# Performance work log

Hardware: AMD Instinct MI355X
Metric: run time of the kernel (lower is better)

The kernel has to match this reference:

```python
import jax, jax.numpy as jnp
import numpy as np

B, S, D_IN, D_OUT = 8, 1024, 4096, 4096

def setup_inputs() -> dict:
    key = jax.random.key(0)
    k_x, k_wp, k_wn = jax.random.split(key, 3)
    x = jax.random.normal(k_x, (B, S, D_IN), dtype=jnp.float32)
    # nn.Linear weights are [out_features, in_features]
    w_pos = jax.random.normal(k_wp, (D_OUT, D_IN), dtype=jnp.float32) * 0.02
    w_neg = jax.random.normal(k_wn, (D_OUT, D_IN), dtype=jnp.float32) * 0.02
    return {"x": x, "w_pos": w_pos, "w_neg": w_neg}

def reference(x, w_pos, w_neg):
    # Straight-through estimator quantization:
    #   w_pos_quant = (w_pos > 0).float(), gradient flows to w_pos
    #   w_neg_quant = -(w_neg <= 0).float(), gradient flows to w_neg
    wp_q = w_pos + jax.lax.stop_gradient((w_pos > 0).astype(w_pos.dtype) - w_pos)
    wn_q = w_neg + jax.lax.stop_gradient(-(w_neg <= 0).astype(w_neg.dtype) - w_neg)
    # F.linear(x, W) = x @ W.T ; two GEMMs summed
    y_pos = jnp.einsum('bsd,od->bso', x, wp_q)
    y_neg = jnp.einsum('bsd,od->bso', x, wn_q)
    return y_pos + y_neg
```

## Files before the change

kernel.cpp:

```cpp
#include <hip/hip_runtime.h>
#include <hip/hip_bf16.h>
#include <stdint.h>

#define M_TOT 8192
#define N_TOT 4096
#define K_TOT 4096

typedef __bf16 bf16x8 __attribute__((ext_vector_type(8)));
typedef float  f32x4  __attribute__((ext_vector_type(4)));

__device__ __forceinline__ uint16_t f2bf_rne(float f) {
  uint32_t u = __float_as_uint(f);
  u += 0x7fffu + ((u >> 16) & 1u);
  return (uint16_t)(u >> 16);
}

__device__ __forceinline__ uint32_t tern(float p, float n) {
  bool pp = p > 0.0f, nn = n > 0.0f;
  return pp ? (nn ? 0x3F80u : 0u) : (nn ? 0u : 0xBF80u);
}

__global__ __launch_bounds__(256) void cast_x_kernel(const float4* __restrict__ x,
                                                     uint4* __restrict__ out) {
  int t = blockIdx.x * 256 + threadIdx.x;
  float4 a = x[2 * t], b = x[2 * t + 1];
  uint4 o;
  o.x = (uint32_t)f2bf_rne(a.x) | ((uint32_t)f2bf_rne(a.y) << 16);
  o.y = (uint32_t)f2bf_rne(a.z) | ((uint32_t)f2bf_rne(a.w) << 16);
  o.z = (uint32_t)f2bf_rne(b.x) | ((uint32_t)f2bf_rne(b.y) << 16);
  o.w = (uint32_t)f2bf_rne(b.z) | ((uint32_t)f2bf_rne(b.w) << 16);
  out[t] = o;
}

__global__ __launch_bounds__(256) void ternarize_kernel(const float4* __restrict__ wp,
                                                        const float4* __restrict__ wn,
                                                        uint4* __restrict__ out) {
  int t = blockIdx.x * 256 + threadIdx.x;
  float4 p0 = wp[2 * t], p1 = wp[2 * t + 1];
  float4 n0 = wn[2 * t], n1 = wn[2 * t + 1];
  uint4 o;
  o.x = tern(p0.x, n0.x) | (tern(p0.y, n0.y) << 16);
  o.y = tern(p0.z, n0.z) | (tern(p0.w, n0.w) << 16);
  o.z = tern(p1.x, n1.x) | (tern(p1.y, n1.y) << 16);
  o.w = tern(p1.z, n1.z) | (tern(p1.w, n1.w) << 16);
  out[t] = o;
}


#define STAGE_HALF(SP0, SP1, DSTOFF)                                              \
  do {                                                                            \
    __builtin_amdgcn_global_load_lds(                                             \
        (const __attribute__((address_space(1))) unsigned int*)(SP0),             \
        (__attribute__((address_space(3))) unsigned int*)(smem + (DSTOFF) + lds0),\
        16, 0, 0);                                                                \
    __builtin_amdgcn_global_load_lds(                                             \
        (const __attribute__((address_space(1))) unsigned int*)(SP1),             \
        (__attribute__((address_space(3))) unsigned int*)(smem + (DSTOFF) + lds1),\
        16, 0, 0);                                                                \
  } while (0)

__global__ __launch_bounds__(512, 2) void gemm_tern_kernel(const uint16_t* __restrict__ Xb,
                                                           const uint16_t* __restrict__ Wb,
                                                           float* __restrict__ C) {
  __shared__ __align__(16) char smem[131072];
  const int tid  = threadIdx.x;
  const int wave = tid >> 6;
  const int lane = tid & 63;
  const int lh   = lane & 15, lq = lane >> 4;
  const int wm   = wave >> 2;
  const int wn   = wave & 3;

  const int id  = blockIdx.x;
  const int swz = (id & 7) * 64 + (id >> 3);
  const int bn  = swz & 15;
  const int bm  = swz >> 4;

  const int p16 = ((lq ^ ((lh >> 1) & 3)) << 4);
  int aoffs[8], boffs[4];
#pragma unroll
  for (int i = 0; i < 8; ++i) aoffs[i] = (wm * 128 + i * 16 + lh) * 64 + p16;
#pragma unroll
  for (int j = 0; j < 4; ++j) boffs[j] = 65536 + (wn * 64 + j * 16 + lh) * 64 + p16;

  const int lds0 = wave * 2048;
  const int lds1 = lds0 + 1024;
  const char *srcA0, *srcA1, *srcB0, *srcB1;
  {
    int o0 = lds0 + lane * 16, o1 = lds1 + lane * 16;
    int r0 = o0 >> 6, r1 = o1 >> 6;
    int c0 = ((o0 >> 4) & 3) ^ ((r0 >> 1) & 3);
    int c1 = ((o1 >> 4) & 3) ^ ((r1 >> 1) & 3);
    srcA0 = (const char*)Xb + (size_t)(bm * 256 + r0) * (K_TOT * 2) + c0 * 16;
    srcA1 = (const char*)Xb + (size_t)(bm * 256 + r1) * (K_TOT * 2) + c1 * 16;
    srcB0 = (const char*)Wb + (size_t)(bn * 256 + r0) * (K_TOT * 2) + c0 * 16;
    srcB1 = (const char*)Wb + (size_t)(bn * 256 + r1) * (K_TOT * 2) + c1 * 16;
  }

  f32x4 acc[8][4];
#pragma unroll
  for (int i = 0; i < 8; ++i)
#pragma unroll
    for (int j = 0; j < 4; ++j) acc[i][j] = (f32x4){0.f, 0.f, 0.f, 0.f};

  STAGE_HALF(srcA0, srcA1, 0);
  STAGE_HALF(srcB0, srcB1, 65536);
  STAGE_HALF(srcA0 + 64, srcA1 + 64, 32768);
  STAGE_HALF(srcB0 + 64, srcB1 + 64, 98304);
  STAGE_HALF(srcA0 + 128, srcA1 + 128, 16384);
  STAGE_HALF(srcB0 + 128, srcB1 + 128, 81920);
  asm volatile("s_waitcnt vmcnt(4)" ::: "memory");
  __builtin_amdgcn_s_barrier();
  asm volatile("" ::: "memory");

  for (int t = 0; t < 64; ++t) {
    const int curb = (t & 1) * 16384;
    const int nxtb = 16384 - curb;
    int offk1 = t * 128 + 192; if (offk1 > 8128) offk1 = 8128;
    int offk0 = t * 128 + 256; if (offk0 > 8128) offk0 = 8128;
    bf16x8 af[4], bfr[4];

#pragma unroll
    for (int i = 0; i < 4; ++i) af[i] = *(const bf16x8*)(smem + aoffs[i]);
#pragma unroll
    for (int j = 0; j < 4; ++j) bfr[j] = *(const bf16x8*)(smem + boffs[j]);
    STAGE_HALF(srcA0 + offk1, srcA1 + offk1, nxtb + 32768);
    __builtin_amdgcn_s_barrier();
    asm volatile("s_waitcnt lgkmcnt(0)" ::: "memory");
    __builtin_amdgcn_sched_barrier(0);
    __builtin_amdgcn_s_setprio(1);
#pragma unroll
    for (int i = 0; i < 4; ++i)
#pragma unroll
      for (int j = 0; j < 4; ++j)
        acc[i][j] = __builtin_amdgcn_mfma_f32_16x16x32_bf16(af[i], bfr[j], acc[i][j], 0, 0, 0);
    __builtin_amdgcn_s_setprio(0);
    __builtin_amdgcn_sched_barrier(0);
    __builtin_amdgcn_s_barrier();
    asm volatile("" ::: "memory");

#pragma unroll
    for (int i = 0; i < 4; ++i) af[i] = *(const bf16x8*)(smem + aoffs[4 + i]);
    STAGE_HALF(srcB0 + offk1, srcB1 + offk1, 98304 + nxtb);
    __builtin_amdgcn_s_barrier();
    asm volatile("s_waitcnt lgkmcnt(0)" ::: "memory");
    __builtin_amdgcn_sched_barrier(0);
    __builtin_amdgcn_s_setprio(1);
#pragma unroll
    for (int i = 0; i < 4; ++i)
#pragma unroll
      for (int j = 0; j < 4; ++j)
        acc[4 + i][j] = __builtin_amdgcn_mfma_f32_16x16x32_bf16(af[i], bfr[j], acc[4 + i][j], 0, 0, 0);
    __builtin_amdgcn_s_setprio(0);
    asm volatile("s_waitcnt vmcnt(8)" ::: "memory");
    __builtin_amdgcn_sched_barrier(0);
    __builtin_amdgcn_s_barrier();
    asm volatile("" ::: "memory");

#pragma unroll
    for (int i = 0; i < 4; ++i) af[i] = *(const bf16x8*)(smem + aoffs[i] + 32768);
#pragma unroll
    for (int j = 0; j < 4; ++j) bfr[j] = *(const bf16x8*)(smem + boffs[j] + 32768);
    STAGE_HALF(srcA0 + offk0, srcA1 + offk0, curb);
    __builtin_amdgcn_s_barrier();
    asm volatile("s_waitcnt lgkmcnt(0)" ::: "memory");
    __builtin_amdgcn_sched_barrier(0);
    __builtin_amdgcn_s_setprio(1);
#pragma unroll
    for (int i = 0; i < 4; ++i)
#pragma unroll
      for (int j = 0; j < 4; ++j)
        acc[i][j] = __builtin_amdgcn_mfma_f32_16x16x32_bf16(af[i], bfr[j], acc[i][j], 0, 0, 0);
    __builtin_amdgcn_s_setprio(0);
    __builtin_amdgcn_sched_barrier(0);
    __builtin_amdgcn_s_barrier();
    asm volatile("" ::: "memory");

#pragma unroll
    for (int i = 0; i < 4; ++i) af[i] = *(const bf16x8*)(smem + aoffs[4 + i] + 32768);
    STAGE_HALF(srcB0 + offk0, srcB1 + offk0, 65536 + curb);
    __builtin_amdgcn_s_barrier();
    asm volatile("s_waitcnt lgkmcnt(0)" ::: "memory");
    __builtin_amdgcn_sched_barrier(0);
    __builtin_amdgcn_s_setprio(1);
#pragma unroll
    for (int i = 0; i < 4; ++i)
#pragma unroll
      for (int j = 0; j < 4; ++j)
        acc[4 + i][j] = __builtin_amdgcn_mfma_f32_16x16x32_bf16(af[i], bfr[j], acc[4 + i][j], 0, 0, 0);
    __builtin_amdgcn_s_setprio(0);
    asm volatile("s_waitcnt vmcnt(8)" ::: "memory");
    __builtin_amdgcn_sched_barrier(0);
    __builtin_amdgcn_s_barrier();
    asm volatile("" ::: "memory");

#pragma unroll
    for (int i = 0; i < 8; ++i) aoffs[i] ^= 16384;
#pragma unroll
    for (int j = 0; j < 4; ++j) boffs[j] ^= 16384;
  }

  asm volatile("s_waitcnt vmcnt(0)" ::: "memory");

  const size_t base_m = (size_t)bm * 256 + wm * 128;
  const size_t base_n = (size_t)bn * 256 + wn * 64;
#pragma unroll
  for (int i = 0; i < 8; ++i) {
#pragma unroll
    for (int j = 0; j < 4; ++j) {
      size_t m0 = base_m + i * 16 + lq * 4;
      size_t n  = base_n + j * 16 + lh;
      float* p = C + m0 * N_TOT + n;
#pragma unroll
      for (int r = 0; r < 4; ++r) p[(size_t)r * N_TOT] = acc[i][j][r];
    }
  }
}

extern "C" void kernel_launch(void* const* d_in, const int* in_sizes, int n_in,
                              void* d_out, int out_size, void* d_ws, size_t ws_size,
                              hipStream_t stream) {
  const float* x  = (const float*)d_in[0];
  const float* wp = (const float*)d_in[1];
  const float* wn = (const float*)d_in[2];
  float* y = (float*)d_out;

  uint16_t* Xb = (uint16_t*)d_ws;
  uint16_t* Wb = Xb + (size_t)M_TOT * K_TOT;

  cast_x_kernel<<<(M_TOT * (size_t)K_TOT) / 2048, 256, 0, stream>>>(
      (const float4*)x, (uint4*)Xb);
  ternarize_kernel<<<(N_TOT * (size_t)K_TOT) / 2048, 256, 0, stream>>>(
      (const float4*)wp, (const float4*)wn, (uint4*)Wb);

  gemm_tern_kernel<<<dim3(512), dim3(512), 0, stream>>>(Xb, Wb, y);
}
```

Measured before the change: 531.4 us.

## Software-pipeline LDS fragment reads across MFMA phases and merge prep kernels

Restructures the GEMM main loop so each phase's LDS fragment loads for the next MFMA block are issued before the current MFMA block runs. LDS read latency is hidden behind matrix math instead of stalling on lgkmcnt(0) before every MFMA group. The vmcnt waits are retuned to match, and source pointers are reworked as a base plus 32-bit offsets. The two preprocessing kernels (bf16 cast of x and ternarization of the weights) are fused into one launch. The cost is higher register pressure from six fragment buffers, and a risk of LDS hazards, since the lgkmcnt waits are now implicit.

```diff
diff --git a/kernel.cpp b/kernel.cpp
--- a/kernel.cpp
+++ b/kernel.cpp
@@ -20,44 +20,47 @@
   return pp ? (nn ? 0x3F80u : 0u) : (nn ? 0u : 0xBF80u);
 }
 
-__global__ __launch_bounds__(256) void cast_x_kernel(const float4* __restrict__ x,
-                                                     uint4* __restrict__ out) {
-  int t = blockIdx.x * 256 + threadIdx.x;
-  float4 a = x[2 * t], b = x[2 * t + 1];
-  uint4 o;
-  o.x = (uint32_t)f2bf_rne(a.x) | ((uint32_t)f2bf_rne(a.y) << 16);
-  o.y = (uint32_t)f2bf_rne(a.z) | ((uint32_t)f2bf_rne(a.w) << 16);
-  o.z = (uint32_t)f2bf_rne(b.x) | ((uint32_t)f2bf_rne(b.y) << 16);
-  o.w = (uint32_t)f2bf_rne(b.z) | ((uint32_t)f2bf_rne(b.w) << 16);
-  out[t] = o;
-}
-
-__global__ __launch_bounds__(256) void ternarize_kernel(const float4* __restrict__ wp,
-                                                        const float4* __restrict__ wn,
-                                                        uint4* __restrict__ out) {
-  int t = blockIdx.x * 256 + threadIdx.x;
-  float4 p0 = wp[2 * t], p1 = wp[2 * t + 1];
-  float4 n0 = wn[2 * t], n1 = wn[2 * t + 1];
-  uint4 o;
-  o.x = tern(p0.x, n0.x) | (tern(p0.y, n0.y) << 16);
-  o.y = tern(p0.z, n0.z) | (tern(p0.w, n0.w) << 16);
-  o.z = tern(p1.x, n1.x) | (tern(p1.y, n1.y) << 16);
-  o.w = tern(p1.z, n1.z) | (tern(p1.w, n1.w) << 16);
-  out[t] = o;
-}
-
-
-#define STAGE_HALF(SP0, SP1, DSTOFF)                                              \
-  do {                                                                            \
-    __builtin_amdgcn_global_load_lds(                                             \
-        (const __attribute__((address_space(1))) unsigned int*)(SP0),             \
-        (__attribute__((address_space(3))) unsigned int*)(smem + (DSTOFF) + lds0),\
-        16, 0, 0);                                                                \
-    __builtin_amdgcn_global_load_lds(                                             \
-        (const __attribute__((address_space(1))) unsigned int*)(SP1),             \
-        (__attribute__((address_space(3))) unsigned int*)(smem + (DSTOFF) + lds1),\
-        16, 0, 0);                                                                \
+__global__ __launch_bounds__(256) void prep_kernel(const float4* __restrict__ x,
+                                                   uint4* __restrict__ Xb4,
+                                                   const float4* __restrict__ wp,
+                                                   const float4* __restrict__ wn,
+                                                   uint4* __restrict__ Wb4) {
+  int b = blockIdx.x;
+  if (b < 16384) {
+    int t = b * 256 + (int)threadIdx.x;
+    float4 a = x[2 * t], c = x[2 * t + 1];
+    uint4 o;
+    o.x = (uint32_t)f2bf_rne(a.x) | ((uint32_t)f2bf_rne(a.y) << 16);
+    o.y = (uint32_t)f2bf_rne(a.z) | ((uint32_t)f2bf_rne(a.w) << 16);
+    o.z = (uint32_t)f2bf_rne(c.x) | ((uint32_t)f2bf_rne(c.y) << 16);
+    o.w = (uint32_t)f2bf_rne(c.z) | ((uint32_t)f2bf_rne(c.w) << 16);
+    Xb4[t] = o;
+  } else {
+    int t = (b - 16384) * 256 + (int)threadIdx.x;
+    float4 p0 = wp[2 * t], p1 = wp[2 * t + 1];
+    float4 n0 = wn[2 * t], n1 = wn[2 * t + 1];
+    uint4 o;
+    o.x = tern(p0.x, n0.x) | (tern(p0.y, n0.y) << 16);
+    o.y = tern(p0.z, n0.z) | (tern(p0.w, n0.w) << 16);
+    o.z = tern(p1.x, n1.x) | (tern(p1.y, n1.y) << 16);
+    o.w = tern(p1.z, n1.z) | (tern(p1.w, n1.w) << 16);
+    Wb4[t] = o;
+  }
+}
+
+
+#define GLDS(SRC, DST)                                                        \
+  __builtin_amdgcn_global_load_lds(                                           \
+      (const __attribute__((address_space(1))) unsigned int*)(SRC),           \
+      (__attribute__((address_space(3))) unsigned int*)(DST), 16, 0, 0)
+
+#define STAGE_HALF(BASE, OFF, DSTOFF)                                         \
+  do {                                                                        \
+    GLDS((BASE) + loff0 + (OFF), smem + (DSTOFF) + lds0);                     \
+    GLDS((BASE) + loff1 + (OFF), smem + (DSTOFF) + lds1);                     \
   } while (0)
+
+#define FENCE() asm volatile("" ::: "memory")
 
 __global__ __launch_bounds__(512, 2) void gemm_tern_kernel(const uint16_t* __restrict__ Xb,
                                                            const uint16_t* __restrict__ Wb,
@@ -84,17 +87,17 @@
 
   const int lds0 = wave * 2048;
   const int lds1 = lds0 + 1024;
-  const char *srcA0, *srcA1, *srcB0, *srcB1;
+  uint32_t loff0, loff1;
   {
     int o0 = lds0 + lane * 16, o1 = lds1 + lane * 16;
     int r0 = o0 >> 6, r1 = o1 >> 6;
     int c0 = ((o0 >> 4) & 3) ^ ((r0 >> 1) & 3);
     int c1 = ((o1 >> 4) & 3) ^ ((r1 >> 1) & 3);
-    srcA0 = (const char*)Xb + (size_t)(bm * 256 + r0) * (K_TOT * 2) + c0 * 16;
-    srcA1 = (const char*)Xb + (size_t)(bm * 256 + r1) * (K_TOT * 2) + c1 * 16;
-    srcB0 = (const char*)Wb + (size_t)(bn * 256 + r0) * (K_TOT * 2) + c0 * 16;
-    srcB1 = (const char*)Wb + (size_t)(bn * 256 + r1) * (K_TOT * 2) + c1 * 16;
-  }
+    loff0 = (uint32_t)r0 * (K_TOT * 2) + (uint32_t)c0 * 16;
+    loff1 = (uint32_t)r1 * (K_TOT * 2) + (uint32_t)c1 * 16;
+  }
+  const char* Abase = (const char*)Xb + (size_t)bm * 256 * (K_TOT * 2);
+  const char* Bbase = (const char*)Wb + (size_t)bn * 256 * (K_TOT * 2);
 
   f32x4 acc[8][4];
 #pragma unroll
@@ -102,96 +105,93 @@
 #pragma unroll
     for (int j = 0; j < 4; ++j) acc[i][j] = (f32x4){0.f, 0.f, 0.f, 0.f};
 
-  STAGE_HALF(srcA0, srcA1, 0);
-  STAGE_HALF(srcB0, srcB1, 65536);
-  STAGE_HALF(srcA0 + 64, srcA1 + 64, 32768);
-  STAGE_HALF(srcB0 + 64, srcB1 + 64, 98304);
-  STAGE_HALF(srcA0 + 128, srcA1 + 128, 16384);
-  STAGE_HALF(srcB0 + 128, srcB1 + 128, 81920);
+  STAGE_HALF(Abase, 0, 0);
+  STAGE_HALF(Bbase, 0, 65536);
+  STAGE_HALF(Abase, 64, 32768);
+  STAGE_HALF(Bbase, 64, 98304);
+  STAGE_HALF(Abase, 128, 16384);
+  STAGE_HALF(Bbase, 128, 81920);
   asm volatile("s_waitcnt vmcnt(4)" ::: "memory");
   __builtin_amdgcn_s_barrier();
-  asm volatile("" ::: "memory");
+  FENCE();
+
+  bf16x8 a0[4], a1[4], a2[4], a3[4], b0[4], b1[4];
+#pragma unroll
+  for (int i = 0; i < 4; ++i) a0[i] = *(const bf16x8*)(smem + aoffs[i]);
+#pragma unroll
+  for (int j = 0; j < 4; ++j) b0[j] = *(const bf16x8*)(smem + boffs[j]);
 
   for (int t = 0; t < 64; ++t) {
     const int curb = (t & 1) * 16384;
     const int nxtb = 16384 - curb;
     int offk1 = t * 128 + 192; if (offk1 > 8128) offk1 = 8128;
     int offk0 = t * 128 + 256; if (offk0 > 8128) offk0 = 8128;
-    bf16x8 af[4], bfr[4];
-
-#pragma unroll
-    for (int i = 0; i < 4; ++i) af[i] = *(const bf16x8*)(smem + aoffs[i]);
-#pragma unroll
-    for (int j = 0; j < 4; ++j) bfr[j] = *(const bf16x8*)(smem + boffs[j]);
-    STAGE_HALF(srcA0 + offk1, srcA1 + offk1, nxtb + 32768);
-    __builtin_amdgcn_s_barrier();
-    asm volatile("s_waitcnt lgkmcnt(0)" ::: "memory");
-    __builtin_amdgcn_sched_barrier(0);
-    __builtin_amdgcn_s_setprio(1);
-#pragma unroll
-    for (int i = 0; i < 4; ++i)
-#pragma unroll
-      for (int j = 0; j < 4; ++j)
-        acc[i][j] = __builtin_amdgcn_mfma_f32_16x16x32_bf16(af[i], bfr[j], acc[i][j], 0, 0, 0);
-    __builtin_amdgcn_s_setprio(0);
-    __builtin_amdgcn_sched_barrier(0);
-    __builtin_amdgcn_s_barrier();
-    asm volatile("" ::: "memory");
-
-#pragma unroll
-    for (int i = 0; i < 4; ++i) af[i] = *(const bf16x8*)(smem + aoffs[4 + i]);
-    STAGE_HALF(srcB0 + offk1, srcB1 + offk1, 98304 + nxtb);
-    __builtin_amdgcn_s_barrier();
-    asm volatile("s_waitcnt lgkmcnt(0)" ::: "memory");
-    __builtin_amdgcn_sched_barrier(0);
-    __builtin_amdgcn_s_setprio(1);
-#pragma unroll
-    for (int i = 0; i < 4; ++i)
-#pragma unroll
-      for (int j = 0; j < 4; ++j)
-        acc[4 + i][j] = __builtin_amdgcn_mfma_f32_16x16x32_bf16(af[i], bfr[j], acc[4 + i][j], 0, 0, 0);
-    __builtin_amdgcn_s_setprio(0);
-    asm volatile("s_waitcnt vmcnt(8)" ::: "memory");
-    __builtin_amdgcn_sched_barrier(0);
-    __builtin_amdgcn_s_barrier();
-    asm volatile("" ::: "memory");
-
-#pragma unroll
-    for (int i = 0; i < 4; ++i) af[i] = *(const bf16x8*)(smem + aoffs[i] + 32768);
-#pragma unroll
-    for (int j = 0; j < 4; ++j) bfr[j] = *(const bf16x8*)(smem + boffs[j] + 32768);
-    STAGE_HALF(srcA0 + offk0, srcA1 + offk0, curb);
-    __builtin_amdgcn_s_barrier();
-    asm volatile("s_waitcnt lgkmcnt(0)" ::: "memory");
-    __builtin_amdgcn_sched_barrier(0);
-    __builtin_amdgcn_s_setprio(1);
-#pragma unroll
-    for (int i = 0; i < 4; ++i)
-#pragma unroll
-      for (int j = 0; j < 4; ++j)
-        acc[i][j] = __builtin_amdgcn_mfma_f32_16x16x32_bf16(af[i], bfr[j], acc[i][j], 0, 0, 0);
-    __builtin_amdgcn_s_setprio(0);
-    __builtin_amdgcn_sched_barrier(0);
-    __builtin_amdgcn_s_barrier();
-    asm volatile("" ::: "memory");
-
-#pragma unroll
-    for (int i = 0; i < 4; ++i) af[i] = *(const bf16x8*)(smem + aoffs[4 + i] + 32768);
-    STAGE_HALF(srcB0 + offk0, srcB1 + offk0, 65536 + curb);
-    __builtin_amdgcn_s_barrier();
-    asm volatile("s_waitcnt lgkmcnt(0)" ::: "memory");
-    __builtin_amdgcn_sched_barrier(0);
-    __builtin_amdgcn_s_setprio(1);
-#pragma unroll
-    for (int i = 0; i < 4; ++i)
-#pragma unroll
-      for (int j = 0; j < 4; ++j)
-        acc[4 + i][j] = __builtin_amdgcn_mfma_f32_16x16x32_bf16(af[i], bfr[j], acc[4 + i][j], 0, 0, 0);
-    __builtin_amdgcn_s_setprio(0);
-    asm volatile("s_waitcnt vmcnt(8)" ::: "memory");
-    __builtin_amdgcn_sched_barrier(0);
-    __builtin_amdgcn_s_barrier();
-    asm volatile("" ::: "memory");
+
+    STAGE_HALF(Abase, offk1, nxtb + 32768);
+    __builtin_amdgcn_s_barrier();
+    FENCE();
+#pragma unroll
+    for (int i = 0; i < 4; ++i) a1[i] = *(const bf16x8*)(smem + aoffs[4 + i]);
+    __builtin_amdgcn_s_setprio(1);
+#pragma unroll
+    for (int i = 0; i < 4; ++i)
+#pragma unroll
+      for (int j = 0; j < 4; ++j)
+        acc[i][j] = __builtin_amdgcn_mfma_f32_16x16x32_bf16(a0[i], b0[j], acc[i][j], 0, 0, 0);
+    __builtin_amdgcn_s_setprio(0);
+    asm volatile("s_waitcnt vmcnt(6)" ::: "memory");
+    __builtin_amdgcn_s_barrier();
+    FENCE();
+
+    STAGE_HALF(Bbase, offk1, nxtb + 98304);
+    __builtin_amdgcn_s_barrier();
+    FENCE();
+#pragma unroll
+    for (int i = 0; i < 4; ++i) a2[i] = *(const bf16x8*)(smem + aoffs[i] + 32768);
+#pragma unroll
+    for (int j = 0; j < 4; ++j) b1[j] = *(const bf16x8*)(smem + boffs[j] + 32768);
+    __builtin_amdgcn_s_setprio(1);
+#pragma unroll
+    for (int i = 0; i < 4; ++i)
+#pragma unroll
+      for (int j = 0; j < 4; ++j)
+        acc[4 + i][j] = __builtin_amdgcn_mfma_f32_16x16x32_bf16(a1[i], b0[j], acc[4 + i][j], 0, 0, 0);
+    __builtin_amdgcn_s_setprio(0);
+    __builtin_amdgcn_s_barrier();
+    FENCE();
+
+    STAGE_HALF(Abase, offk0, curb);
+    __builtin_amdgcn_s_barrier();
+    FENCE();
+#pragma unroll
+    for (int i = 0; i < 4; ++i) a3[i] = *(const bf16x8*)(smem + aoffs[4 + i] + 32768);
+    __builtin_amdgcn_s_setprio(1);
+#pragma unroll
+    for (int i = 0; i < 4; ++i)
+#pragma unroll
+      for (int j = 0; j < 4; ++j)
+        acc[i][j] = __builtin_amdgcn_mfma_f32_16x16x32_bf16(a2[i], b1[j], acc[i][j], 0, 0, 0);
+    __builtin_amdgcn_s_setprio(0);
+    asm volatile("s_waitcnt vmcnt(6)" ::: "memory");
+    __builtin_amdgcn_s_barrier();
+    FENCE();
+
+    STAGE_HALF(Bbase, offk0, 65536 + curb);
+    __builtin_amdgcn_s_barrier();
+    FENCE();
+#pragma unroll
+    for (int i = 0; i < 4; ++i) a0[i] = *(const bf16x8*)(smem + (aoffs[i] ^ 16384));
+#pragma unroll
+    for (int j = 0; j < 4; ++j) b0[j] = *(const bf16x8*)(smem + (boffs[j] ^ 16384));
+    __builtin_amdgcn_s_setprio(1);
+#pragma unroll
+    for (int i = 0; i < 4; ++i)
+#pragma unroll
+      for (int j = 0; j < 4; ++j)
+        acc[4 + i][j] = __builtin_amdgcn_mfma_f32_16x16x32_bf16(a3[i], b1[j], acc[4 + i][j], 0, 0, 0);
+    __builtin_amdgcn_s_setprio(0);
+    __builtin_amdgcn_s_barrier();
+    FENCE();
 
 #pragma unroll
     for (int i = 0; i < 8; ++i) aoffs[i] ^= 16384;
@@ -227,10 +227,9 @@
   uint16_t* Xb = (uint16_t*)d_ws;
   uint16_t* Wb = Xb + (size_t)M_TOT * K_TOT;
 
-  cast_x_kernel<<<(M_TOT * (size_t)K_TOT) / 2048, 256, 0, stream>>>(
-      (const float4*)x, (uint4*)Xb);
-  ternarize_kernel<<<(N_TOT * (size_t)K_TOT) / 2048, 256, 0, stream>>>(
-      (const float4*)wp, (const float4*)wn, (uint4*)Wb);
+  prep_kernel<<<24576, 256, 0, stream>>>((const float4*)x, (uint4*)Xb,
+                                         (const float4*)wp, (const float4*)wn,
+                                         (uint4*)Wb);
 
   gemm_tern_kernel<<<dim3(512), dim3(512), 0, stream>>>(Xb, Wb, y);
 }
```

Result: no change. 526.9 us (-0.8%).
